# Kernel optimization log

Hardware: AMD Instinct MI355X
Metric: run time of the kernel (lower is better)

Reference implementation:

```python
import jax, jax.numpy as jnp
import numpy as np


def setup_inputs() -> dict:
    key = jax.random.key(0)
    ks = jax.random.split(key, 12)
    N_DRUGS, D, N_CELLS, C_IN, E = 4096, 128, 1024, 1000, 500000
    inp = {
        "drug_hidden_out": jax.random.normal(ks[0], (N_DRUGS, D), dtype=jnp.float32),
        "cell_hidden_out": jax.random.normal(ks[1], (N_CELLS, C_IN), dtype=jnp.float32),
        # columns: drug1_idx, drug2_idx, cell_idx, label (original code indexes
        # drug_hidden_out with ALL THREE index columns, so bound by N_DRUGS)
        "all_edges": jax.random.randint(ks[2], (E, 4), 0, N_DRUGS, dtype=jnp.int64),
        # proj: Linear(1000, 128)
        "proj_W": jax.random.normal(ks[3], (D, C_IN), dtype=jnp.float32) * 0.03,
        "proj_b": jnp.zeros((D,), dtype=jnp.float32),
        # NN: Linear(128,32) -> ReLU -> Linear(32,32) -> ReLU -> Linear(32,32)
        #     -> ReLU -> Dropout(eval=identity) -> Linear(32,1) -> Sigmoid
        "W1": jax.random.normal(ks[4], (32, D), dtype=jnp.float32) * 0.08,
        "b1": jnp.zeros((32,), dtype=jnp.float32),
        "W2": jax.random.normal(ks[5], (32, 32), dtype=jnp.float32) * 0.17,
        "b2": jnp.zeros((32,), dtype=jnp.float32),
        "W3": jax.random.normal(ks[6], (32, 32), dtype=jnp.float32) * 0.17,
        "b3": jnp.zeros((32,), dtype=jnp.float32),
        "W4": jax.random.normal(ks[7], (1, 32), dtype=jnp.float32) * 0.17,
        "b4": jnp.zeros((1,), dtype=jnp.float32),
    }
    return inp


def reference(drug_hidden_out, cell_hidden_out, all_edges,
              proj_W, proj_b, W1, b1, W2, b2, W3, b3, W4, b4):
    # proj is computed in the original forward but its result is never used
    # downstream (the code re-indexes drug_hidden_out for cell_fea).
    _cell_proj = cell_hidden_out @ proj_W.T + proj_b  # [n_cells, 128], dead value

    edges = all_edges.T                 # [4, E]
    label = edges[3]                    # [E]
    edge_index = edges[:3]              # [3, E]

    drug1_fea = drug_hidden_out[edge_index[0]]   # [E, 128] gather
    drug2_fea = drug_hidden_out[edge_index[1]]   # [E, 128] gather
    cell_fea = drug_hidden_out[edge_index[2]]    # [E, 128] gather (faithful to source bug)
    logits = drug1_fea * drug2_fea * cell_fea    # [E, 128]

    h = jax.nn.relu(logits @ W1.T + b1)          # [E, 32]
    h = jax.nn.relu(h @ W2.T + b2)               # [E, 32]
    h = jax.nn.relu(h @ W3.T + b3)               # [E, 32] (dropout = identity in eval)
    x = jax.nn.sigmoid(h @ W4.T + b4)            # [E, 1]
    return x, label
```

## Files before the change

### kernel.cpp

```cpp
#include <hip/hip_runtime.h>
#include <stdint.h>

#define DD 128
#define HH 32
#define RS 40
#define TABQ (4096 * DD / 4)
#define BLOB_OFF (1u << 20)

typedef _Float16 f16;
typedef _Float16 f16x4 __attribute__((ext_vector_type(4)));
typedef _Float16 f16x8 __attribute__((ext_vector_type(8)));
typedef float    f32x4 __attribute__((ext_vector_type(4)));

#define GL1(p)  ((const __attribute__((address_space(1))) void*)(p))
#define LDS3(p) ((__attribute__((address_space(3))) void*)(p))

__global__ __launch_bounds__(256)
void synergy_prepass(const float* __restrict__ drug,
                     const float* __restrict__ W1, const float* __restrict__ W2,
                     const float* __restrict__ W3, f16* __restrict__ tab)
{
    const int tid = threadIdx.x;
    if ((int)blockIdx.x == 512) {
        f16x8* __restrict__ blob16 = (f16x8*)((char*)tab + BLOB_OFF);
        const float4* __restrict__ W1v = (const float4*)W1;
        #pragma unroll
        for (int p = 0; p < 2; ++p) {
            const int S = p * 256 + tid;
            const int t = S >> 8, f = (S >> 6) & 3, l = S & 63;
            const int mm = l & 15, qq = l >> 4;
            const int c4 = (t * 16 + mm) * (DD / 4) + f * 8 + qq * 2;
            const float4 w0 = W1v[c4], w1 = W1v[c4 + 1];
            f16x8 r;
            r[0]=(f16)w0.x; r[1]=(f16)w0.y; r[2]=(f16)w0.z; r[3]=(f16)w0.w;
            r[4]=(f16)w1.x; r[5]=(f16)w1.y; r[6]=(f16)w1.z; r[7]=(f16)w1.w;
            blob16[S] = r;
        }
        {
            const int B = tid & 127;
            const int t = B >> 6, l = B & 63;
            const int mm = l & 15, qq = l >> 4;
            const int c4 = (t * 16 + mm) * (HH / 4) + qq * 2;
            const float4* __restrict__ src = (tid < 128) ? (const float4*)W2 : (const float4*)W3;
            const float4 w0 = src[c4], w1 = src[c4 + 1];
            f16x8 r;
            r[0]=(f16)w0.x; r[1]=(f16)w0.y; r[2]=(f16)w0.z; r[3]=(f16)w0.w;
            r[4]=(f16)w1.x; r[5]=(f16)w1.y; r[6]=(f16)w1.z; r[7]=(f16)w1.w;
            blob16[512 + (tid & 128) + B] = r;
        }
        return;
    }
    const int i = blockIdx.x * 256 + tid;
    if (i < TABQ) {
        const float4 v = ((const float4*)drug)[i];
        f16x4 h;
        h[0]=(f16)v.x; h[1]=(f16)v.y; h[2]=(f16)v.z; h[3]=(f16)v.w;
        ((f16x4*)tab)[i] = h;
    }
}

__global__ __launch_bounds__(256, 3)
void synergy_main(const f16* __restrict__ tab, const int* __restrict__ edges,
                  const float* __restrict__ W4, const float* __restrict__ b1,
                  const float* __restrict__ b2, const float* __restrict__ b3,
                  const float* __restrict__ b4, float* __restrict__ out, int E)
{
    __shared__ __align__(16) f16 stage[4][6144];

    const int tid  = threadIdx.x;
    const int wave = tid >> 6;
    const int lane = tid & 63;
    const int m    = lane & 15;
    const int q    = lane >> 4;

    const int waveBase = blockIdx.x * 64 + wave * 16;
    const char* __restrict__ tabB = (const char*)tab;

    const f16x8* __restrict__ blobG = (const f16x8*)(tabB + BLOB_OFF);
    f16x8 wa[2][4];
    #pragma unroll
    for (int t = 0; t < 2; ++t)
        #pragma unroll
        for (int f = 0; f < 4; ++f)
            wa[t][f] = blobG[(t * 4 + f) * 64 + lane];
    const f16x8 w2a = blobG[512 + lane], w2b = blobG[576 + lane];
    const f16x8 w3a = blobG[640 + lane], w3b = blobG[704 + lane];
    const float b1a = b1[m], b1b = b1[16 + m];
    const float b2a = b2[m], b2b = b2[16 + m];
    const float b3a = b3[m], b3b = b3[16 + m];
    const float w4a = W4[m], w4b = W4[16 + m];
    const float b4v = b4[0];

    int eL = waveBase + m;
    eL = (eL < E) ? eL : (E - 1);
    const int4 ed = ((const int4*)edges)[eL];

    if (lane < 16 && waveBase + lane < E)
        out[E + waveBase + lane] = (float)ed.w;

    int rowb[12];
    #pragma unroll
    for (int g = 0; g < 4; ++g) {
        const int src = 4 * g + q;
        rowb[0 * 4 + g] = __shfl(ed.x, src, 64) << 8;
        rowb[1 * 4 + g] = __shfl(ed.y, src, 64) << 8;
        rowb[2 * 4 + g] = __shfl(ed.z, src, 64) << 8;
    }

    f16* __restrict__ stg = stage[wave];
    #pragma unroll
    for (int t = 0; t < 3; ++t)
        #pragma unroll
        for (int g = 0; g < 4; ++g) {
            const int seg = (m + 4 * g + q) & 15;
            __builtin_amdgcn_global_load_lds(
                GL1(tabB + (size_t)(rowb[t * 4 + g] + (seg << 4))),
                LDS3((char*)stg + (t * 16 + 4 * g) * 256), 16, 0, 0);
        }
    __builtin_amdgcn_sched_barrier(0);
    __builtin_amdgcn_s_waitcnt(0x0F70);
    __builtin_amdgcn_sched_barrier(0);

    f32x4 acc0 = {b1a, b1a, b1a, b1a};
    f32x4 acc1 = {b1b, b1b, b1b, b1b};
    #pragma unroll
    for (int f = 0; f < 4; ++f) {
        const int slot = (((f * 4 + q) - m) & 15) << 3;
        const f16x8 v0 = *(const f16x8*)(stg + (0 * 16 + m) * 128 + slot);
        const f16x8 v1 = *(const f16x8*)(stg + (1 * 16 + m) * 128 + slot);
        const f16x8 v2 = *(const f16x8*)(stg + (2 * 16 + m) * 128 + slot);
        const f16x8 p = v0 * v1 * v2;
        acc0 = __builtin_amdgcn_mfma_f32_16x16x32_f16(p, wa[0][f], acc0, 0, 0, 0);
        acc1 = __builtin_amdgcn_mfma_f32_16x16x32_f16(p, wa[1][f], acc1, 0, 0, 0);
    }
    f16* __restrict__ hb = stg;
    #pragma unroll
    for (int r = 0; r < 4; ++r) {
        const int row = 4 * q + r;
        hb[row * RS + m]      = (f16)fmaxf(acc0[r], 0.0f);
        hb[row * RS + 16 + m] = (f16)fmaxf(acc1[r], 0.0f);
    }

    const f16x8 a2 = *(const f16x8*)(hb + m * RS + q * 8);
    f32x4 c0 = {b2a, b2a, b2a, b2a};
    f32x4 c1 = {b2b, b2b, b2b, b2b};
    c0 = __builtin_amdgcn_mfma_f32_16x16x32_f16(a2, w2a, c0, 0, 0, 0);
    c1 = __builtin_amdgcn_mfma_f32_16x16x32_f16(a2, w2b, c1, 0, 0, 0);
    #pragma unroll
    for (int r = 0; r < 4; ++r) {
        const int row = 4 * q + r;
        hb[row * RS + m]      = (f16)fmaxf(c0[r], 0.0f);
        hb[row * RS + 16 + m] = (f16)fmaxf(c1[r], 0.0f);
    }

    const f16x8 a3 = *(const f16x8*)(hb + m * RS + q * 8);
    f32x4 d0 = {b3a, b3a, b3a, b3a};
    f32x4 d1 = {b3b, b3b, b3b, b3b};
    d0 = __builtin_amdgcn_mfma_f32_16x16x32_f16(a3, w3a, d0, 0, 0, 0);
    d1 = __builtin_amdgcn_mfma_f32_16x16x32_f16(a3, w3b, d1, 0, 0, 0);

    float zr[4];
    #pragma unroll
    for (int r = 0; r < 4; ++r)
        zr[r] = fmaxf(d0[r], 0.0f) * w4a + fmaxf(d1[r], 0.0f) * w4b;
    #pragma unroll
    for (int dd = 1; dd < 16; dd <<= 1)
        #pragma unroll
        for (int r = 0; r < 4; ++r)
            zr[r] += __shfl_xor(zr[r], dd, 64);
    if (m == 0) {
        #pragma unroll
        for (int r = 0; r < 4; ++r) {
            const int e = waveBase + 4 * q + r;
            if (e < E) out[e] = 1.0f / (1.0f + __expf(-(zr[r] + b4v)));
        }
    }
}

extern "C" void kernel_launch(void* const* d_in, const int* in_sizes, int n_in,
                              void* d_out, int out_size, void* d_ws, size_t ws_size,
                              hipStream_t stream)
{
    const float* drug  = (const float*)d_in[0];
    const int*   edges = (const int*)d_in[2];
    const float* W1 = (const float*)d_in[5];
    const float* b1 = (const float*)d_in[6];
    const float* W2 = (const float*)d_in[7];
    const float* b2 = (const float*)d_in[8];
    const float* W3 = (const float*)d_in[9];
    const float* b3 = (const float*)d_in[10];
    const float* W4 = (const float*)d_in[11];
    const float* b4 = (const float*)d_in[12];
    float* out = (float*)d_out;
    f16*   tab = (f16*)d_ws;

    const int E = in_sizes[2] / 4;

    hipLaunchKernelGGL(synergy_prepass, dim3(513), dim3(256), 0, stream,
                       drug, W1, W2, W3, tab);
    hipLaunchKernelGGL(synergy_main, dim3((E + 63) / 64), dim3(256), 0, stream,
                       tab, edges, W4, b1, b2, b3, b4, out, E);
}
```

Measured before the change: 125.9 us.

## Make main kernel persistent with software-pipelined gather DMA across edge groups

Converts the main kernel to a persistent grid of at most 768 blocks, where each wave loops over 16-edge groups with a grid stride. Each wave issues the LDS gather DMA for the next group while it computes the later MLP layers of the current group, and it prefetches edge indices two groups ahead. The hidden activations move to a separate small LDS buffer with stride 36 so that reusing the staging buffer does not conflict, and the sigmoid outputs are written as float4. The aim is to hide gather latency and amortize the per-block weight loads, at the cost of fewer resident waves and a serialized loop per wave.

```diff
diff --git a/kernel.cpp b/kernel.cpp
--- a/kernel.cpp
+++ b/kernel.cpp
@@ -3,7 +3,7 @@
 
 #define DD 128
 #define HH 32
-#define RS 40
+#define RS 36
 #define TABQ (4096 * DD / 4)
 #define BLOB_OFF (1u << 20)
 
@@ -63,9 +63,11 @@
 void synergy_main(const f16* __restrict__ tab, const int* __restrict__ edges,
                   const float* __restrict__ W4, const float* __restrict__ b1,
                   const float* __restrict__ b2, const float* __restrict__ b3,
-                  const float* __restrict__ b4, float* __restrict__ out, int E)
+                  const float* __restrict__ b4, float* __restrict__ out,
+                  int E, int NG)
 {
     __shared__ __align__(16) f16 stage[4][6144];
+    __shared__ __align__(16) f16 hbuf[4][16 * RS];
 
     const int tid  = threadIdx.x;
     const int wave = tid >> 6;
@@ -73,8 +75,12 @@
     const int m    = lane & 15;
     const int q    = lane >> 4;
 
-    const int waveBase = blockIdx.x * 64 + wave * 16;
-    const char* __restrict__ tabB = (const char*)tab;
+    const int WSTR = (int)gridDim.x * 4;
+    int g = (int)blockIdx.x * 4 + wave;
+    if (g >= NG) return;
+
+    const char* __restrict__ tabB   = (const char*)tab;
+    const int4* __restrict__ edges4 = (const int4*)edges;
 
     const f16x8* __restrict__ blobG = (const f16x8*)(tabB + BLOB_OFF);
     f16x8 wa[2][4];
@@ -91,89 +97,120 @@
     const float w4a = W4[m], w4b = W4[16 + m];
     const float b4v = b4[0];
 
-    int eL = waveBase + m;
-    eL = (eL < E) ? eL : (E - 1);
-    const int4 ed = ((const int4*)edges)[eL];
-
-    if (lane < 16 && waveBase + lane < E)
-        out[E + waveBase + lane] = (float)ed.w;
-
-    int rowb[12];
-    #pragma unroll
-    for (int g = 0; g < 4; ++g) {
-        const int src = 4 * g + q;
-        rowb[0 * 4 + g] = __shfl(ed.x, src, 64) << 8;
-        rowb[1 * 4 + g] = __shfl(ed.y, src, 64) << 8;
-        rowb[2 * 4 + g] = __shfl(ed.z, src, 64) << 8;
-    }
-
     f16* __restrict__ stg = stage[wave];
-    #pragma unroll
-    for (int t = 0; t < 3; ++t)
-        #pragma unroll
-        for (int g = 0; g < 4; ++g) {
-            const int seg = (m + 4 * g + q) & 15;
-            __builtin_amdgcn_global_load_lds(
-                GL1(tabB + (size_t)(rowb[t * 4 + g] + (seg << 4))),
-                LDS3((char*)stg + (t * 16 + 4 * g) * 256), 16, 0, 0);
-        }
-    __builtin_amdgcn_sched_barrier(0);
-    __builtin_amdgcn_s_waitcnt(0x0F70);
-    __builtin_amdgcn_sched_barrier(0);
-
-    f32x4 acc0 = {b1a, b1a, b1a, b1a};
-    f32x4 acc1 = {b1b, b1b, b1b, b1b};
-    #pragma unroll
-    for (int f = 0; f < 4; ++f) {
-        const int slot = (((f * 4 + q) - m) & 15) << 3;
-        const f16x8 v0 = *(const f16x8*)(stg + (0 * 16 + m) * 128 + slot);
-        const f16x8 v1 = *(const f16x8*)(stg + (1 * 16 + m) * 128 + slot);
-        const f16x8 v2 = *(const f16x8*)(stg + (2 * 16 + m) * 128 + slot);
-        const f16x8 p = v0 * v1 * v2;
-        acc0 = __builtin_amdgcn_mfma_f32_16x16x32_f16(p, wa[0][f], acc0, 0, 0, 0);
-        acc1 = __builtin_amdgcn_mfma_f32_16x16x32_f16(p, wa[1][f], acc1, 0, 0, 0);
-    }
-    f16* __restrict__ hb = stg;
-    #pragma unroll
-    for (int r = 0; r < 4; ++r) {
-        const int row = 4 * q + r;
-        hb[row * RS + m]      = (f16)fmaxf(acc0[r], 0.0f);
-        hb[row * RS + 16 + m] = (f16)fmaxf(acc1[r], 0.0f);
-    }
-
-    const f16x8 a2 = *(const f16x8*)(hb + m * RS + q * 8);
-    f32x4 c0 = {b2a, b2a, b2a, b2a};
-    f32x4 c1 = {b2b, b2b, b2b, b2b};
-    c0 = __builtin_amdgcn_mfma_f32_16x16x32_f16(a2, w2a, c0, 0, 0, 0);
-    c1 = __builtin_amdgcn_mfma_f32_16x16x32_f16(a2, w2b, c1, 0, 0, 0);
-    #pragma unroll
-    for (int r = 0; r < 4; ++r) {
-        const int row = 4 * q + r;
-        hb[row * RS + m]      = (f16)fmaxf(c0[r], 0.0f);
-        hb[row * RS + 16 + m] = (f16)fmaxf(c1[r], 0.0f);
-    }
-
-    const f16x8 a3 = *(const f16x8*)(hb + m * RS + q * 8);
-    f32x4 d0 = {b3a, b3a, b3a, b3a};
-    f32x4 d1 = {b3b, b3b, b3b, b3b};
-    d0 = __builtin_amdgcn_mfma_f32_16x16x32_f16(a3, w3a, d0, 0, 0, 0);
-    d1 = __builtin_amdgcn_mfma_f32_16x16x32_f16(a3, w3b, d1, 0, 0, 0);
-
-    float zr[4];
-    #pragma unroll
-    for (int r = 0; r < 4; ++r)
-        zr[r] = fmaxf(d0[r], 0.0f) * w4a + fmaxf(d1[r], 0.0f) * w4b;
-    #pragma unroll
-    for (int dd = 1; dd < 16; dd <<= 1)
+    f16* __restrict__ hb  = hbuf[wave];
+
+    auto issue_dma = [&](const int4 ed) {
+        #pragma unroll
+        for (int gg = 0; gg < 4; ++gg) {
+            const int src   = 4 * gg + q;
+            const int seg16 = ((m + src) & 15) << 4;
+            const int rx = __shfl(ed.x, src, 64) << 8;
+            __builtin_amdgcn_global_load_lds(GL1(tabB + (size_t)(rx + seg16)),
+                LDS3((char*)stg + (0 * 16 + 4 * gg) * 256), 16, 0, 0);
+            const int ry = __shfl(ed.y, src, 64) << 8;
+            __builtin_amdgcn_global_load_lds(GL1(tabB + (size_t)(ry + seg16)),
+                LDS3((char*)stg + (1 * 16 + 4 * gg) * 256), 16, 0, 0);
+            const int rz = __shfl(ed.z, src, 64) << 8;
+            __builtin_amdgcn_global_load_lds(GL1(tabB + (size_t)(rz + seg16)),
+                LDS3((char*)stg + (2 * 16 + 4 * gg) * 256), 16, 0, 0);
+        }
+    };
+    auto load_ed = [&](int gg) -> int4 {
+        int e = (gg << 4) + m;
+        e = (e < E) ? e : (E - 1);
+        return edges4[e];
+    };
+
+    int4 ed_cur = load_ed(g);
+    issue_dma(ed_cur);
+    int gn = g + WSTR;
+    int4 ed_nxt = load_ed((gn < NG) ? gn : g);
+
+    for (;;) {
+        __builtin_amdgcn_sched_barrier(0);
+        __builtin_amdgcn_s_waitcnt(0x0F70);
+        __builtin_amdgcn_sched_barrier(0);
+
+        f32x4 acc0 = {b1a, b1a, b1a, b1a};
+        f32x4 acc1 = {b1b, b1b, b1b, b1b};
+        #pragma unroll
+        for (int f = 0; f < 4; ++f) {
+            const int slot = (((f * 4 + q) - m) & 15) << 3;
+            const f16x8 v0 = *(const f16x8*)(stg + (0 * 16 + m) * 128 + slot);
+            const f16x8 v1 = *(const f16x8*)(stg + (1 * 16 + m) * 128 + slot);
+            const f16x8 v2 = *(const f16x8*)(stg + (2 * 16 + m) * 128 + slot);
+            const f16x8 p = v0 * v1 * v2;
+            acc0 = __builtin_amdgcn_mfma_f32_16x16x32_f16(p, wa[0][f], acc0, 0, 0, 0);
+            acc1 = __builtin_amdgcn_mfma_f32_16x16x32_f16(p, wa[1][f], acc1, 0, 0, 0);
+        }
+        #pragma unroll
+        for (int r = 0; r < 4; ++r) {
+            const int row = 4 * q + r;
+            hb[row * RS + m]      = (f16)fmaxf(acc0[r], 0.0f);
+            hb[row * RS + 16 + m] = (f16)fmaxf(acc1[r], 0.0f);
+        }
+
+        const int gf = gn + WSTR;
+        const int4 ed_fut = load_ed((gf < NG) ? gf : g);
+
+        if (gn < NG) {
+            __builtin_amdgcn_sched_barrier(0);
+            issue_dma(ed_nxt);
+            __builtin_amdgcn_sched_barrier(0);
+        }
+
+        {
+            const f16x8 a2 = *(const f16x8*)(hb + m * RS + q * 8);
+            f32x4 c0 = {b2a, b2a, b2a, b2a};
+            f32x4 c1 = {b2b, b2b, b2b, b2b};
+            c0 = __builtin_amdgcn_mfma_f32_16x16x32_f16(a2, w2a, c0, 0, 0, 0);
+            c1 = __builtin_amdgcn_mfma_f32_16x16x32_f16(a2, w2b, c1, 0, 0, 0);
+            #pragma unroll
+            for (int r = 0; r < 4; ++r) {
+                const int row = 4 * q + r;
+                hb[row * RS + m]      = (f16)fmaxf(c0[r], 0.0f);
+                hb[row * RS + 16 + m] = (f16)fmaxf(c1[r], 0.0f);
+            }
+        }
+
+        f32x4 d0 = {b3a, b3a, b3a, b3a};
+        f32x4 d1 = {b3b, b3b, b3b, b3b};
+        {
+            const f16x8 a3 = *(const f16x8*)(hb + m * RS + q * 8);
+            d0 = __builtin_amdgcn_mfma_f32_16x16x32_f16(a3, w3a, d0, 0, 0, 0);
+            d1 = __builtin_amdgcn_mfma_f32_16x16x32_f16(a3, w3b, d1, 0, 0, 0);
+        }
+
+        float zr[4];
         #pragma unroll
         for (int r = 0; r < 4; ++r)
-            zr[r] += __shfl_xor(zr[r], dd, 64);
-    if (m == 0) {
-        #pragma unroll
-        for (int r = 0; r < 4; ++r) {
-            const int e = waveBase + 4 * q + r;
-            if (e < E) out[e] = 1.0f / (1.0f + __expf(-(zr[r] + b4v)));
-        }
+            zr[r] = fmaxf(d0[r], 0.0f) * w4a + fmaxf(d1[r], 0.0f) * w4b;
+        #pragma unroll
+        for (int dd = 1; dd < 16; dd <<= 1)
+            #pragma unroll
+            for (int r = 0; r < 4; ++r)
+                zr[r] += __shfl_xor(zr[r], dd, 64);
+        if (m == 0) {
+            const int e0 = (g << 4) + 4 * q;
+            float4 res;
+            res.x = 1.0f / (1.0f + __expf(-(zr[0] + b4v)));
+            res.y = 1.0f / (1.0f + __expf(-(zr[1] + b4v)));
+            res.z = 1.0f / (1.0f + __expf(-(zr[2] + b4v)));
+            res.w = 1.0f / (1.0f + __expf(-(zr[3] + b4v)));
+            if (e0 + 3 < E) *(float4*)(out + e0) = res;
+            else {
+                if (e0 + 0 < E) out[e0 + 0] = res.x;
+                if (e0 + 1 < E) out[e0 + 1] = res.y;
+                if (e0 + 2 < E) out[e0 + 2] = res.z;
+                if (e0 + 3 < E) out[e0 + 3] = res.w;
+            }
+        }
+        const int eL = (g << 4) + lane;
+        if (lane < 16 && eL < E) out[E + eL] = (float)ed_cur.w;
+
+        if (gn >= NG) break;
+        g = gn; gn = gf; ed_cur = ed_nxt; ed_nxt = ed_fut;
     }
 }
 
@@ -194,10 +231,13 @@
     float* out = (float*)d_out;
     f16*   tab = (f16*)d_ws;
 
-    const int E = in_sizes[2] / 4;
+    const int E  = in_sizes[2] / 4;
+    const int NG = (E + 15) / 16;
 
     hipLaunchKernelGGL(synergy_prepass, dim3(513), dim3(256), 0, stream,
                        drug, W1, W2, W3, tab);
-    hipLaunchKernelGGL(synergy_main, dim3((E + 63) / 64), dim3(256), 0, stream,
-                       tab, edges, W4, b1, b2, b3, b4, out, E);
+    int blocks = (NG + 3) / 4;
+    if (blocks > 768) blocks = 768;
+    hipLaunchKernelGGL(synergy_main, dim3(blocks), dim3(256), 0, stream,
+                       tab, edges, W4, b1, b2, b3, b4, out, E, NG);
 }
```

Measured after the change: 123.7 us. No clear change (-1.8%).
